# Performance work log

Hardware: AMD Instinct MI355X
Metric: run time of the kernel (lower is better)

The kernel has to match this reference:

```python
import jax, jax.numpy as jnp
import numpy as np

NUM_EXPERTS = 8
IN_FEATURES = 1024
HIDDEN_FEATURES = 4096
OUT_FEATURES = 1024
TOKENS = 8192


def setup_inputs() -> dict:
    key = jax.random.key(0)
    k_x, k_idx, k_w1, k_w2, k_b1, k_b2 = jax.random.split(key, 6)
    x = jax.random.normal(k_x, (TOKENS, IN_FEATURES), dtype=jnp.float32)
    indices_s = jax.random.randint(k_idx, (TOKENS,), 0, NUM_EXPERTS, dtype=jnp.int64)
    # learned parameters (torch uses torch.rand; scaled for numeric sanity)
    weight1 = jax.random.normal(k_w1, (NUM_EXPERTS, IN_FEATURES, HIDDEN_FEATURES), dtype=jnp.float32) * 0.02
    weight2 = jax.random.normal(k_w2, (NUM_EXPERTS, HIDDEN_FEATURES, OUT_FEATURES), dtype=jnp.float32) * 0.02
    bias1 = jax.random.normal(k_b1, (NUM_EXPERTS, HIDDEN_FEATURES), dtype=jnp.float32) * 0.02
    bias2 = jax.random.normal(k_b2, (NUM_EXPERTS, IN_FEATURES), dtype=jnp.float32) * 0.02
    return {"x": x, "indices_s": indices_s, "weight1": weight1, "weight2": weight2, "bias1": bias1, "bias2": bias2}


def reference(x, indices_s, weight1, weight2, bias1, bias2):
    # Per-token expert MLP. Rather than gathering full weight matrices per
    # token (weight[indices_s] -> [T, in, hid], huge), loop over the small
    # fixed expert set and mask-combine. Math identical to the torch module.
    T = x.shape[0]
    num_experts = weight1.shape[0]
    out = jnp.zeros((T, weight2.shape[2]), dtype=x.dtype)
    for e in range(num_experts):
        mask = (indices_s == e)[:, None]  # [T, 1]
        h = jax.nn.gelu(x @ weight1[e] + bias1[e], approximate=False)  # [T, hid]
        y = h @ weight2[e] + bias2[e]  # [T, out]
        out = out + jnp.where(mask, y, jnp.zeros((), dtype=x.dtype))
    # original returns shape [T, 1, out] (x was unsqueezed)
    return out[:, None, :]
```

## Files before the change

### kernel.cpp

```cpp
#include <hip/hip_runtime.h>
#include <hip/hip_bf16.h>
#include <math.h>

#define TOKENS 8192
#define IN_F   1024
#define HID_F  4096
#define OUT_F  1024
#define NEXP   8
#define TSLOTS 40

typedef __attribute__((ext_vector_type(8))) short bf16x8;
typedef __attribute__((ext_vector_type(4))) float f32x4;
typedef __attribute__((ext_vector_type(8))) unsigned short u16x8;

__device__ __forceinline__ unsigned short f2bf(float f) {
    unsigned int u = __float_as_uint(f);
    u += 0x7fffu + ((u >> 16) & 1u);
    return (unsigned short)(u >> 16);
}

__device__ __forceinline__ void gload_lds16(const unsigned short* g, unsigned char* lds) {
    __builtin_amdgcn_global_load_lds(
        (const __attribute__((address_space(1))) void*)g,
        (__attribute__((address_space(3))) void*)lds, 16, 0, 0);
}

__global__ void sort_kernel(const int* __restrict__ idx, int* __restrict__ perm,
                            int* __restrict__ off, int* __restrict__ table) {
    __shared__ int cnt[NEXP];
    __shared__ int base[NEXP];
    const int tid = threadIdx.x, lane = tid & 63;
    if (tid < NEXP) cnt[tid] = 0;
    __syncthreads();
    for (int i = tid; i < TOKENS; i += 1024) {
        int e = idx[i];
#pragma unroll
        for (int ex = 0; ex < NEXP; ++ex) {
            unsigned long long m = __ballot(e == ex);
            if (lane == 0 && m) atomicAdd(&cnt[ex], __popcll(m));
        }
    }
    __syncthreads();
    if (tid == 0) {
        int s = 0;
        for (int e = 0; e < NEXP; ++e) { off[e] = s; base[e] = s; s += cnt[e]; }
        off[NEXP] = s;
        int t = 0;
        for (int e = 0; e < NEXP; ++e)
            for (int m0 = off[e]; m0 < off[e + 1]; m0 += 256)
                table[t++] = (e << 13) | m0;
        for (; t < TSLOTS; ++t) table[t] = -1;
    }
    __syncthreads();
    for (int i = tid; i < TOKENS; i += 1024) {
        int e = idx[i];
#pragma unroll
        for (int ex = 0; ex < NEXP; ++ex) {
            unsigned long long m = __ballot(e == ex);
            if (e == ex) {
                int lead = (int)__ffsll((long long)m) - 1;
                int pos = 0;
                if (lane == lead) pos = atomicAdd(&base[ex], __popcll(m));
                pos = __shfl(pos, lead);
                pos += __popcll(m & ((1ULL << lane) - 1ULL));
                perm[pos] = i;
            }
        }
    }
}

__device__ __forceinline__ void transp_tile(const float* __restrict__ in,
                                            unsigned short* __restrict__ out,
                                            int R, int C, int e, int by, int bx,
                                            unsigned short* T, int st) {
    const int r0 = by * 64, c0 = bx * 64;
    const int rr = st >> 4, cc = st & 15;
    const float* ip = in + ((size_t)e * R + r0) * C + c0;
#pragma unroll
    for (int p = 0; p < 4; ++p) {
        int r = p * 16 + rr;
        float4 v = *(const float4*)(ip + (size_t)r * C + cc * 4);
        T[(cc * 4 + 0) * 65 + r] = f2bf(v.x);
        T[(cc * 4 + 1) * 65 + r] = f2bf(v.y);
        T[(cc * 4 + 2) * 65 + r] = f2bf(v.z);
        T[(cc * 4 + 3) * 65 + r] = f2bf(v.w);
    }
    __syncthreads();
    unsigned short* op = out + ((size_t)e * C + c0) * R + r0;
    const int c = st >> 2, ch = st & 3;
    u16x8 a, b;
#pragma unroll
    for (int i = 0; i < 8; ++i) a[i] = T[c * 65 + ch * 16 + i];
#pragma unroll
    for (int i = 0; i < 8; ++i) b[i] = T[c * 65 + ch * 16 + 8 + i];
    *(u16x8*)(op + (size_t)c * R + ch * 16) = a;
    *(u16x8*)(op + (size_t)c * R + ch * 16 + 8) = b;
}

__global__ void transp(const float* __restrict__ in, unsigned short* __restrict__ out,
                       int R, int C) {
    __shared__ unsigned short T[64 * 65];
    transp_tile(in, out, R, C, blockIdx.z, blockIdx.y, blockIdx.x, T, threadIdx.x);
}

__global__ void fused_pre(const float* __restrict__ x, const int* __restrict__ perm,
                          unsigned short* __restrict__ xg,
                          const float* __restrict__ w1, unsigned short* __restrict__ w1t) {
    __shared__ unsigned short T[64 * 65];
    const int bid = blockIdx.x, t = threadIdx.x;
    if (bid < TOKENS) {
        const int src = perm[bid];
        float4 v = *(const float4*)(x + (size_t)src * IN_F + t * 4);
        unsigned long long pk =
            (unsigned long long)f2bf(v.x) |
            ((unsigned long long)f2bf(v.y) << 16) |
            ((unsigned long long)f2bf(v.z) << 32) |
            ((unsigned long long)f2bf(v.w) << 48);
        *(unsigned long long*)(xg + (size_t)bid * IN_F + t * 4) = pk;
        return;
    }
    const int id = bid - TOKENS;
    const int e = id >> 10, rem = id & 1023;
    const int by = rem >> 6, bx = rem & 63;
    transp_tile(w1, w1t, IN_F, HID_F, e, by, bx, T, t);
}

#define RD_A(RB, HALF) \
  _Pragma("unroll") for (int m_ = 0; m_ < 4; ++m_) { \
    const int row_ = wr * 128 + (HALF) * 64 + m_ * 16 + lr; \
    _Pragma("unroll") for (int kk_ = 0; kk_ < 2; ++kk_) \
      aR[m_][kk_] = *(const bf16x8*)((RB) + row_ * 128 + (((kk_ * 4 + hk) << 4) ^ xorc)); }

#define RD_B(RB, NH, DST) \
  _Pragma("unroll") for (int nn_ = 0; nn_ < 2; ++nn_) { \
    const int row_ = wc * 64 + ((NH) * 2 + nn_) * 16 + lr; \
    _Pragma("unroll") for (int kk_ = 0; kk_ < 2; ++kk_) \
      DST[nn_][kk_] = *(const bf16x8*)((RB) + 32768 + row_ * 128 + (((kk_ * 4 + hk) << 4) ^ xorc)); }

#define MFMA_Q(MH, NH, B) \
  __builtin_amdgcn_s_setprio(1); \
  _Pragma("unroll") for (int m_ = 0; m_ < 4; ++m_) \
    _Pragma("unroll") for (int nn_ = 0; nn_ < 2; ++nn_) \
      _Pragma("unroll") for (int kk_ = 0; kk_ < 2; ++kk_) \
        acc[(MH) * 4 + m_][(NH) * 2 + nn_] = __builtin_amdgcn_mfma_f32_16x16x32_bf16( \
            aR[m_][kk_], B[nn_][kk_], acc[(MH) * 4 + m_][(NH) * 2 + nn_], 0, 0, 0); \
  __builtin_amdgcn_s_setprio(0);

template<int K, int ND, bool GELU>
__launch_bounds__(512, 2)
__global__ void moe_gemm8p(const unsigned short* __restrict__ A,
                           const unsigned short* __restrict__ W,
                           const float* __restrict__ bias,
                           const int* __restrict__ perm,
                           const int* __restrict__ off,
                           const int* __restrict__ table,
                           void* __restrict__ outp,
                           const float* __restrict__ w2src,
                           unsigned short* __restrict__ w2t) {
    const int nwg = (ND / 256) * TSLOTS;

    __shared__ __align__(16) unsigned char L[131072];
    const int tid = threadIdx.x;

    if ((int)blockIdx.x >= nwg) {
        const int sub = tid >> 8, st = tid & 255;
        const int id2 = ((int)blockIdx.x - nwg) * 2 + sub;
        const int e = id2 >> 10, rem = id2 & 1023;
        const int by = rem >> 4, bx = rem & 15;
        unsigned short* T = (unsigned short*)(L + sub * 8448);
        transp_tile(w2src, w2t, HID_F, OUT_F, e, by, bx, T, st);
        return;
    }

    const int chunk = nwg >> 3;
    const int logical = ((int)blockIdx.x & 7) * chunk + ((int)blockIdx.x >> 3);
    const int pr   = logical / (2 * TSLOTS);
    const int rem2 = logical - pr * (2 * TSLOTS);
    const int ts = rem2 >> 1;
    const int nt = pr * 2 + (rem2 & 1);
    const int te = table[ts];
    if (te < 0) return;
    const int e  = te >> 13;
    const int m0 = te & 8191;
    const int sege = off[e + 1];
    const int n0 = nt * 256;

    const int wid = tid >> 6, lane = tid & 63;
    const int wr = wid >> 2, wc = wid & 3;
    const int lr = lane & 15, hk = lane >> 4;

    const unsigned short* We = W + (size_t)e * ND * K + (size_t)n0 * K;

    const int srow8 = lane >> 3;
    const int sch   = (lane & 7) ^ srow8;
    const unsigned short* aSrc[4];
    const unsigned short* wSrc[4];
#pragma unroll
    for (int cc = 0; cc < 4; ++cc) {
        int rt = cc * 64 + wid * 8 + srow8;
        int ga = m0 + rt; if (ga > TOKENS - 1) ga = TOKENS - 1;
        aSrc[cc] = A  + (size_t)ga * K + sch * 8;
        wSrc[cc] = We + (size_t)rt * K + sch * 8;
    }
    const int dstBase = wid * 1024;

    constexpr int NT = K / 64;

    auto stageH = [&](int tile, int h) {
        const int buf = (tile & 1) * 65536;
        const int op  = (h >> 1) * 32768;
        const int c0_ = (h & 1) * 2;
        const int ko  = tile * 64;
#pragma unroll
        for (int j = 0; j < 2; ++j) {
            int cc = c0_ + j;
            const unsigned short* s = (h < 2) ? (aSrc[cc] + ko) : (wSrc[cc] + ko);
            gload_lds16(s, L + buf + op + cc * 8192 + dstBase);
        }
    };

    f32x4 acc[8][4];
#pragma unroll
    for (int i = 0; i < 8; ++i)
#pragma unroll
        for (int j = 0; j < 4; ++j) acc[i][j] = (f32x4){0.f, 0.f, 0.f, 0.f};

    bf16x8 aR[4][2], b0R[2][2], b1R[2][2];
    const int xorc = (lr & 7) << 4;
    const unsigned char* rb0 = L;
    const unsigned char* rb1 = L + 65536;

    stageH(0, 0); stageH(0, 1); stageH(0, 2); stageH(0, 3);
    stageH(1, 0);
    asm volatile("s_waitcnt vmcnt(2)" ::: "memory");
    __builtin_amdgcn_s_barrier();
    __builtin_amdgcn_sched_barrier(0);

#pragma unroll 1
    for (int i = 0; i < NT / 2; ++i) {
        const int T1 = 2 * i + 1;
        const bool lastIt = (i == NT / 2 - 1);
        RD_A(rb0, 0); RD_B(rb0, 0, b0R);
        stageH(T1, 1);
        __builtin_amdgcn_s_barrier();
        MFMA_Q(0, 0, b0R);
        __builtin_amdgcn_s_barrier();
        RD_B(rb0, 1, b1R);
        stageH(T1, 2);
        __builtin_amdgcn_s_barrier();
        MFMA_Q(0, 1, b1R);
        __builtin_amdgcn_s_barrier();
        RD_A(rb0, 1);
        stageH(T1, 3);
        __builtin_amdgcn_s_barrier();
        MFMA_Q(1, 1, b1R);
        __builtin_amdgcn_s_barrier();
        if (!lastIt) stageH(T1 + 1, 0);
        __builtin_amdgcn_s_barrier();
        MFMA_Q(1, 0, b0R);
        if (lastIt) { asm volatile("s_waitcnt vmcnt(0)" ::: "memory"); }
        else        { asm volatile("s_waitcnt vmcnt(2)" ::: "memory"); }
        __builtin_amdgcn_s_barrier();
        __builtin_amdgcn_sched_barrier(0);
        RD_A(rb1, 0); RD_B(rb1, 0, b0R);
        if (!lastIt) stageH(T1 + 1, 1);
        __builtin_amdgcn_s_barrier();
        MFMA_Q(0, 0, b0R);
        __builtin_amdgcn_s_barrier();
        RD_B(rb1, 1, b1R);
        if (!lastIt) stageH(T1 + 1, 2);
        __builtin_amdgcn_s_barrier();
        MFMA_Q(0, 1, b1R);
        __builtin_amdgcn_s_barrier();
        RD_A(rb1, 1);
        if (!lastIt) stageH(T1 + 1, 3);
        __builtin_amdgcn_s_barrier();
        MFMA_Q(1, 1, b1R);
        __builtin_amdgcn_s_barrier();
        if (!lastIt) stageH(T1 + 2, 0);
        __builtin_amdgcn_s_barrier();
        MFMA_Q(1, 0, b0R);
        if (!lastIt) { asm volatile("s_waitcnt vmcnt(2)" ::: "memory"); }
        __builtin_amdgcn_s_barrier();
        __builtin_amdgcn_sched_barrier(0);
    }

    const float* be = bias + (size_t)e * ND + n0;
#pragma unroll
    for (int m = 0; m < 8; ++m) {
#pragma unroll
        for (int r = 0; r < 4; ++r) {
            int row = wr * 128 + m * 16 + hk * 4 + r;
            int grow = m0 + row;
            if (grow >= sege) continue;
            if constexpr (GELU) {
                unsigned short* h = (unsigned short*)outp;
                size_t base = (size_t)grow * ND + n0;
#pragma unroll
                for (int n = 0; n < 4; ++n) {
                    int col = wc * 64 + n * 16 + lr;
                    float v = acc[m][n][r] + be[col];
                    float u = v * (0.7978845608f + 0.0356774081f * v * v);
                    float g = v / (1.0f + __expf(-2.0f * u));
                    h[base + col] = f2bf(g);
                }
            } else {
                float* out = (float*)outp;
                int tok = perm[grow];
                size_t base = (size_t)tok * ND + n0;
#pragma unroll
                for (int n = 0; n < 4; ++n) {
                    int col = wc * 64 + n * 16 + lr;
                    out[base + col] = acc[m][n][r] + be[col];
                }
            }
        }
    }
}

extern "C" void kernel_launch(void* const* d_in, const int* in_sizes, int n_in,
                              void* d_out, int out_size, void* d_ws, size_t ws_size,
                              hipStream_t stream) {
    const float* x   = (const float*)d_in[0];
    const int*   idx = (const int*)d_in[1];
    const float* w1  = (const float*)d_in[2];
    const float* w2  = (const float*)d_in[3];
    const float* b1  = (const float*)d_in[4];
    const float* b2  = (const float*)d_in[5];
    float* out = (float*)d_out;

    int* perm  = (int*)d_ws;
    int* off   = perm + TOKENS;
    int* table = off + 16;
    unsigned short* xg  = (unsigned short*)((char*)d_ws + 65536);
    unsigned short* h   = xg + (size_t)TOKENS * IN_F;
    unsigned short* w1t = h + (size_t)TOKENS * HID_F;
    unsigned short* w2t = w1t + (size_t)NEXP * IN_F * HID_F;
    const size_t need_fused = 65536
        + (size_t)TOKENS * IN_F * 2
        + (size_t)TOKENS * HID_F * 2
        + (size_t)NEXP * IN_F * HID_F * 2 * 2;
    const bool fused = (ws_size >= need_fused);

    hipLaunchKernelGGL(sort_kernel, dim3(1), dim3(1024), 0, stream, idx, perm, off, table);
    hipLaunchKernelGGL(fused_pre, dim3(TOKENS + NEXP * (IN_F / 64) * (HID_F / 64)),
                       dim3(256), 0, stream, x, perm, xg, w1, w1t);

    const int g1 = (HID_F / 256) * TSLOTS;
    const int t2 = NEXP * (OUT_F / 64) * (HID_F / 64) / 2;
    if (fused) {
        hipLaunchKernelGGL((moe_gemm8p<IN_F, HID_F, true>), dim3(g1 + t2), dim3(512),
                           0, stream, xg, w1t, b1, perm, off, table, (void*)h, w2, w2t);
        hipLaunchKernelGGL((moe_gemm8p<HID_F, OUT_F, false>),
                           dim3((OUT_F / 256) * TSLOTS), dim3(512),
                           0, stream, h, w2t, b2, perm, off, table, (void*)out,
                           (const float*)nullptr, (unsigned short*)nullptr);
    } else {
        hipLaunchKernelGGL((moe_gemm8p<IN_F, HID_F, true>), dim3(g1), dim3(512),
                           0, stream, xg, w1t, b1, perm, off, table, (void*)h,
                           (const float*)nullptr, (unsigned short*)nullptr);
        hipLaunchKernelGGL(transp, dim3(OUT_F / 64, HID_F / 64, NEXP), dim3(256), 0, stream,
                           w2, w1t, HID_F, OUT_F);
        hipLaunchKernelGGL((moe_gemm8p<HID_F, OUT_F, false>),
                           dim3((OUT_F / 256) * TSLOTS), dim3(512),
                           0, stream, h, w1t, b2, perm, off, table, (void*)out,
                           (const float*)nullptr, (unsigned short*)nullptr);
    }
}
```

Before: 312.8 us.

## Software-pipeline LDS fragment reads one quadrant ahead across tile boundaries

Restructures the GEMM main loop so the A/B register fragments for the next quadrant, including the first quadrant of the next tile, are read from LDS before the current MFMA quadrant runs. The last quadrant of each tile now overlaps with the LDS reads and global staging for the next tile. A second A register set and extra B buffers are added, and one more staging chunk is issued in the prologue. The goal is to hide LDS read latency behind MFMA work, at the cost of higher register pressure under launch_bounds(512,2) and a more intricate barrier and waitcnt schedule.

Result: slower. 833.3 us (+166.4%).

```diff
diff --git a/kernel.cpp b/kernel.cpp
--- a/kernel.cpp
+++ b/kernel.cpp
@@ -125,11 +125,11 @@
     transp_tile(w1, w1t, IN_F, HID_F, e, by, bx, T, t);
 }
 
-#define RD_A(RB, HALF) \
+#define RD_A2(RB, HALF, DST) \
   _Pragma("unroll") for (int m_ = 0; m_ < 4; ++m_) { \
     const int row_ = wr * 128 + (HALF) * 64 + m_ * 16 + lr; \
     _Pragma("unroll") for (int kk_ = 0; kk_ < 2; ++kk_) \
-      aR[m_][kk_] = *(const bf16x8*)((RB) + row_ * 128 + (((kk_ * 4 + hk) << 4) ^ xorc)); }
+      DST[m_][kk_] = *(const bf16x8*)((RB) + row_ * 128 + (((kk_ * 4 + hk) << 4) ^ xorc)); }
 
 #define RD_B(RB, NH, DST) \
   _Pragma("unroll") for (int nn_ = 0; nn_ < 2; ++nn_) { \
@@ -137,13 +137,13 @@
     _Pragma("unroll") for (int kk_ = 0; kk_ < 2; ++kk_) \
       DST[nn_][kk_] = *(const bf16x8*)((RB) + 32768 + row_ * 128 + (((kk_ * 4 + hk) << 4) ^ xorc)); }
 
-#define MFMA_Q(MH, NH, B) \
+#define MFMA_Q2(MH, NH, AREG, BREG) \
   __builtin_amdgcn_s_setprio(1); \
   _Pragma("unroll") for (int m_ = 0; m_ < 4; ++m_) \
     _Pragma("unroll") for (int nn_ = 0; nn_ < 2; ++nn_) \
       _Pragma("unroll") for (int kk_ = 0; kk_ < 2; ++kk_) \
         acc[(MH) * 4 + m_][(NH) * 2 + nn_] = __builtin_amdgcn_mfma_f32_16x16x32_bf16( \
-            aR[m_][kk_], B[nn_][kk_], acc[(MH) * 4 + m_][(NH) * 2 + nn_], 0, 0, 0); \
+            AREG[m_][kk_], BREG[nn_][kk_], acc[(MH) * 4 + m_][(NH) * 2 + nn_], 0, 0, 0); \
   __builtin_amdgcn_s_setprio(0);
 
 template<int K, int ND, bool GELU>
@@ -225,64 +225,67 @@
 #pragma unroll
         for (int j = 0; j < 4; ++j) acc[i][j] = (f32x4){0.f, 0.f, 0.f, 0.f};
 
-    bf16x8 aR[4][2], b0R[2][2], b1R[2][2];
+    bf16x8 a0r[4][2], a1r[4][2], bE[2][2], bS[2][2], bO[2][2];
     const int xorc = (lr & 7) << 4;
     const unsigned char* rb0 = L;
     const unsigned char* rb1 = L + 65536;
 
     stageH(0, 0); stageH(0, 1); stageH(0, 2); stageH(0, 3);
-    stageH(1, 0);
-    asm volatile("s_waitcnt vmcnt(2)" ::: "memory");
+    stageH(1, 0); stageH(1, 1);
+    asm volatile("s_waitcnt vmcnt(4)" ::: "memory");
     __builtin_amdgcn_s_barrier();
     __builtin_amdgcn_sched_barrier(0);
+    RD_A2(rb0, 0, a0r); RD_B(rb0, 0, bE);
 
 #pragma unroll 1
     for (int i = 0; i < NT / 2; ++i) {
         const int T1 = 2 * i + 1;
         const bool lastIt = (i == NT / 2 - 1);
-        RD_A(rb0, 0); RD_B(rb0, 0, b0R);
-        stageH(T1, 1);
-        __builtin_amdgcn_s_barrier();
-        MFMA_Q(0, 0, b0R);
-        __builtin_amdgcn_s_barrier();
-        RD_B(rb0, 1, b1R);
+        RD_B(rb0, 1, bS);
         stageH(T1, 2);
         __builtin_amdgcn_s_barrier();
-        MFMA_Q(0, 1, b1R);
-        __builtin_amdgcn_s_barrier();
-        RD_A(rb0, 1);
+        MFMA_Q2(0, 0, a0r, bE);
+        __builtin_amdgcn_s_barrier();
+        RD_A2(rb0, 1, a1r);
         stageH(T1, 3);
         __builtin_amdgcn_s_barrier();
-        MFMA_Q(1, 1, b1R);
+        MFMA_Q2(0, 1, a0r, bS);
         __builtin_amdgcn_s_barrier();
         if (!lastIt) stageH(T1 + 1, 0);
         __builtin_amdgcn_s_barrier();
-        MFMA_Q(1, 0, b0R);
+        MFMA_Q2(1, 1, a1r, bS);
         if (lastIt) { asm volatile("s_waitcnt vmcnt(0)" ::: "memory"); }
         else        { asm volatile("s_waitcnt vmcnt(2)" ::: "memory"); }
         __builtin_amdgcn_s_barrier();
         __builtin_amdgcn_sched_barrier(0);
-        RD_A(rb1, 0); RD_B(rb1, 0, b0R);
+        RD_A2(rb1, 0, a0r); RD_B(rb1, 0, bO);
         if (!lastIt) stageH(T1 + 1, 1);
         __builtin_amdgcn_s_barrier();
-        MFMA_Q(0, 0, b0R);
-        __builtin_amdgcn_s_barrier();
-        RD_B(rb1, 1, b1R);
+        MFMA_Q2(1, 0, a1r, bE);
+        __builtin_amdgcn_s_barrier();
+        RD_B(rb1, 1, bS);
         if (!lastIt) stageH(T1 + 1, 2);
         __builtin_amdgcn_s_barrier();
-        MFMA_Q(0, 1, b1R);
-        __builtin_amdgcn_s_barrier();
-        RD_A(rb1, 1);
+        MFMA_Q2(0, 0, a0r, bO);
+        __builtin_amdgcn_s_barrier();
+        RD_A2(rb1, 1, a1r);
         if (!lastIt) stageH(T1 + 1, 3);
         __builtin_amdgcn_s_barrier();
-        MFMA_Q(1, 1, b1R);
+        MFMA_Q2(0, 1, a0r, bS);
         __builtin_amdgcn_s_barrier();
         if (!lastIt) stageH(T1 + 2, 0);
         __builtin_amdgcn_s_barrier();
-        MFMA_Q(1, 0, b0R);
+        MFMA_Q2(1, 1, a1r, bS);
         if (!lastIt) { asm volatile("s_waitcnt vmcnt(2)" ::: "memory"); }
         __builtin_amdgcn_s_barrier();
         __builtin_amdgcn_sched_barrier(0);
+        if (!lastIt) {
+            RD_A2(rb0, 0, a0r); RD_B(rb0, 0, bE);
+            stageH(T1 + 2, 1);
+        }
+        __builtin_amdgcn_s_barrier();
+        MFMA_Q2(1, 0, a1r, bO);
+        __builtin_amdgcn_s_barrier();
     }
 
     const float* be = bias + (size_t)e * ND + n0;
```

## Overlap expert sort with W1 transpose and split token gather into own kernel

Applied to the files above, without the earlier changes.

The single-block sort kernel is folded into the W1 transpose/convert kernel as block 0, running with 256 threads, so sorting overlaps with the weight transpose instead of serialising before it. The token gather and bf16 conversion move into a separate kernel launched after, because it depends on the sort's permutation. The launch count stays the same, but the sort now runs with a quarter of the threads and could become the tail of that kernel.

Measured after the change: 350.8 us. 12.2% more time.

```diff
diff --git a/kernel.cpp b/kernel.cpp
--- a/kernel.cpp
+++ b/kernel.cpp
@@ -25,14 +25,14 @@
         (__attribute__((address_space(3))) void*)lds, 16, 0, 0);
 }
 
-__global__ void sort_kernel(const int* __restrict__ idx, int* __restrict__ perm,
-                            int* __restrict__ off, int* __restrict__ table) {
+__device__ void sort_body(const int* __restrict__ idx, int* __restrict__ perm,
+                          int* __restrict__ off, int* __restrict__ table) {
     __shared__ int cnt[NEXP];
     __shared__ int base[NEXP];
     const int tid = threadIdx.x, lane = tid & 63;
     if (tid < NEXP) cnt[tid] = 0;
     __syncthreads();
-    for (int i = tid; i < TOKENS; i += 1024) {
+    for (int i = tid; i < TOKENS; i += 256) {
         int e = idx[i];
 #pragma unroll
         for (int ex = 0; ex < NEXP; ++ex) {
@@ -52,7 +52,7 @@
         for (; t < TSLOTS; ++t) table[t] = -1;
     }
     __syncthreads();
-    for (int i = tid; i < TOKENS; i += 1024) {
+    for (int i = tid; i < TOKENS; i += 256) {
         int e = idx[i];
 #pragma unroll
         for (int ex = 0; ex < NEXP; ++ex) {
@@ -103,26 +103,30 @@
     transp_tile(in, out, R, C, blockIdx.z, blockIdx.y, blockIdx.x, T, threadIdx.x);
 }
 
-__global__ void fused_pre(const float* __restrict__ x, const int* __restrict__ perm,
-                          unsigned short* __restrict__ xg,
-                          const float* __restrict__ w1, unsigned short* __restrict__ w1t) {
+__global__ void pre_sort_w1t(const int* __restrict__ idx, int* __restrict__ perm,
+                             int* __restrict__ off, int* __restrict__ table,
+                             const float* __restrict__ w1,
+                             unsigned short* __restrict__ w1t) {
+    const int bid = blockIdx.x;
+    if (bid == 0) { sort_body(idx, perm, off, table); return; }
     __shared__ unsigned short T[64 * 65];
-    const int bid = blockIdx.x, t = threadIdx.x;
-    if (bid < TOKENS) {
-        const int src = perm[bid];
-        float4 v = *(const float4*)(x + (size_t)src * IN_F + t * 4);
-        unsigned long long pk =
-            (unsigned long long)f2bf(v.x) |
-            ((unsigned long long)f2bf(v.y) << 16) |
-            ((unsigned long long)f2bf(v.z) << 32) |
-            ((unsigned long long)f2bf(v.w) << 48);
-        *(unsigned long long*)(xg + (size_t)bid * IN_F + t * 4) = pk;
-        return;
-    }
-    const int id = bid - TOKENS;
+    const int id = bid - 1;
     const int e = id >> 10, rem = id & 1023;
     const int by = rem >> 6, bx = rem & 63;
-    transp_tile(w1, w1t, IN_F, HID_F, e, by, bx, T, t);
+    transp_tile(w1, w1t, IN_F, HID_F, e, by, bx, T, threadIdx.x);
+}
+
+__global__ void gather_x(const float* __restrict__ x, const int* __restrict__ perm,
+                         unsigned short* __restrict__ xg) {
+    const int row = blockIdx.x, t = threadIdx.x;
+    const int src = perm[row];
+    float4 v = *(const float4*)(x + (size_t)src * IN_F + t * 4);
+    unsigned long long pk =
+        (unsigned long long)f2bf(v.x) |
+        ((unsigned long long)f2bf(v.y) << 16) |
+        ((unsigned long long)f2bf(v.z) << 32) |
+        ((unsigned long long)f2bf(v.w) << 48);
+    *(unsigned long long*)(xg + (size_t)row * IN_F + t * 4) = pk;
 }
 
 #define RD_A(RB, HALF) \
@@ -342,9 +346,9 @@
         + (size_t)NEXP * IN_F * HID_F * 2 * 2;
     const bool fused = (ws_size >= need_fused);
 
-    hipLaunchKernelGGL(sort_kernel, dim3(1), dim3(1024), 0, stream, idx, perm, off, table);
-    hipLaunchKernelGGL(fused_pre, dim3(TOKENS + NEXP * (IN_F / 64) * (HID_F / 64)),
-                       dim3(256), 0, stream, x, perm, xg, w1, w1t);
+    hipLaunchKernelGGL(pre_sort_w1t, dim3(1 + NEXP * (IN_F / 64) * (HID_F / 64)),
+                       dim3(256), 0, stream, idx, perm, off, table, w1, w1t);
+    hipLaunchKernelGGL(gather_x, dim3(TOKENS), dim3(256), 0, stream, x, perm, xg);
 
     const int g1 = (HID_F / 256) * TSLOTS;
     const int t2 = NEXP * (OUT_F / 64) * (HID_F / 64) / 2;
```
